# Performance work log

Hardware: AMD Instinct MI355X
Metric: run time of the kernel (lower is better)

The kernel has to match this reference:

```python
import jax, jax.numpy as jnp
import numpy as np

P = 8          # patch_size
DIM = 256      # embed dim
HEADS = 8
HEAD_DIM = DIM // HEADS
CH = 3
PATCH_DIM = CH * P * P  # 192
INNER = int(4.0 * DIM)  # 1024
SCALE = HEAD_DIM ** -0.5


def sine_pos_embedding(n, c, dtype=jnp.float32):
    # standard 1D sinusoidal position encoding, shape (n, c)
    pos = jnp.arange(n, dtype=jnp.float32)[:, None]            # (n,1)
    div = jnp.exp(jnp.arange(0, c, 2, dtype=jnp.float32) * (-np.log(10000.0) / c))
    pe = jnp.zeros((n, c), dtype=jnp.float32)
    pe = pe.at[:, 0::2].set(jnp.sin(pos * div))
    pe = pe.at[:, 1::2].set(jnp.cos(pos * div))
    return pe.astype(dtype)


def patchify(x):
    # (B,C,H,W) -> (B, n, p1*p2*C), matching 'b c (h p1) (w p2) -> b (h w) (p1 p2 c)'
    B, C, H, W = x.shape
    hp, wp = H // P, W // P
    x = x.reshape(B, C, hp, P, wp, P)
    x = x.transpose(0, 2, 4, 3, 5, 1)        # (B, hp, wp, p1, p2, C)
    return x.reshape(B, hp * wp, P * P * C)


def unpatchify(x, hp, wp):
    # (B, n, p1*p2*C) -> (B, C, H, W)
    B = x.shape[0]
    x = x.reshape(B, hp, wp, P, P, CH)
    x = x.transpose(0, 5, 1, 3, 2, 4)        # (B, C, hp, p1, wp, p2)
    return x.reshape(B, CH, hp * P, wp * P)


def setup_inputs() -> dict:
    key = jax.random.key(0)
    ks = jax.random.split(key, 16)
    B, H, W = 8, 256, 256
    s = 0.02
    img0 = jax.random.normal(ks[0], (B, CH, H, W), dtype=jnp.float32)
    img1 = jax.random.normal(ks[1], (B, CH, H, W), dtype=jnp.float32)
    mask = jax.random.randint(ks[2], (B, 1, H, W), 0, 2).astype(jnp.float32)
    return {
        "img0": img0,
        "img1": img1,
        "mask": mask,
        "w_patch": jax.random.normal(ks[3], (PATCH_DIM, DIM), jnp.float32) * s,
        "b_patch": jnp.zeros((DIM,), jnp.float32),
        "w_kv": jax.random.normal(ks[4], (DIM, 2 * DIM), jnp.float32) * s,
        "b_kv": jnp.zeros((2 * DIM,), jnp.float32),
        "w_qv": jax.random.normal(ks[5], (DIM, 2 * DIM), jnp.float32) * s,
        "b_qv": jnp.zeros((2 * DIM,), jnp.float32),
        "w_fc1": jax.random.normal(ks[6], (DIM, INNER), jnp.float32) * s,
        "b_fc1": jnp.zeros((INNER,), jnp.float32),
        "w_fc2": jax.random.normal(ks[7], (INNER, PATCH_DIM), jnp.float32) * s,
        "b_fc2": jnp.zeros((PATCH_DIM,), jnp.float32),
    }


def reference(img0, img1, mask, w_patch, b_patch, w_kv, b_kv, w_qv, b_qv,
              w_fc1, b_fc1, w_fc2, b_fc2):
    B, C, H, W = img0.shape
    hp, wp = H // P, W // P
    n = hp * wp

    x0 = patchify(img0) @ w_patch + b_patch   # (B, n, dim)
    x1 = patchify(img1) @ w_patch + b_patch
    pe = sine_pos_embedding(n, DIM)
    x0 = x0 + pe
    x1 = x1 + pe

    # img0 -> k, v
    kv = (x0 @ w_kv + b_kv).reshape(B, n, 2, HEADS, HEAD_DIM)
    kv = kv.transpose(2, 0, 3, 1, 4)          # (2, B, heads, n, hd)
    k, v = kv[0], kv[1]

    # img1 -> q (v1 unused in forward, matching torch code)
    qv = (x1 @ w_qv + b_qv).reshape(B, n, 2, DIM).transpose(2, 0, 1, 3)
    q = qv[0].reshape(B, n, HEADS, HEAD_DIM).transpose(0, 2, 1, 3)  # (B, heads, n, hd)

    dots = jnp.einsum('bhqd,bhkd->bhqk', q, k) * SCALE  # (B, heads, n, n)

    # mask: (B,1,H,W) -> per-patch sum -> binary -> additive bias over key dim
    msum = mask.reshape(B, 1, hp, P, wp, P).sum(axis=(3, 5)).reshape(B, 1, n)
    bias = jnp.where(msum > 0, 0.0, -100.0)[:, :, None, :]  # (B,1,1,n)

    attn = jax.nn.softmax(dots + bias, axis=-1)
    out = jnp.einsum('bhqk,bhkd->bhqd', attn, v)
    out = out.transpose(0, 2, 1, 3).reshape(B, n, DIM)

    # mlp2: Linear -> GELU(exact) -> Linear
    h = jax.nn.gelu(out @ w_fc1 + b_fc1, approximate=False)
    res = h @ w_fc2 + b_fc2                   # (B, n, patch_dim)

    return unpatchify(res, hp, wp)            # (B, C, H, W)
```

## Files before the change

kernel.cpp:

```cpp
#include <hip/hip_runtime.h>
#include <cstdint>
#include <cstddef>

typedef __bf16 bf16_t;
typedef __bf16 bf16x4 __attribute__((ext_vector_type(4)));
typedef __bf16 bf16x8 __attribute__((ext_vector_type(8)));
typedef float f32x4 __attribute__((ext_vector_type(4)));

__device__ __forceinline__ void gload_lds16(const bf16_t* g, bf16_t* l) {
  __builtin_amdgcn_global_load_lds((const __attribute__((address_space(1))) void*)g,
                                   (__attribute__((address_space(3))) void*)l,
                                   16, 0, 0);
}

__device__ __forceinline__ f32x4 mfma16(bf16x8 a, bf16x8 b, f32x4 c) {
  return __builtin_amdgcn_mfma_f32_16x16x32_bf16(a, b, c, 0, 0, 0);
}

__global__ __launch_bounds__(256)
void prep_all(const float* __restrict__ img0, const float* __restrict__ img1,
              const float* __restrict__ mask,
              const float* __restrict__ wp, const float* __restrict__ wkv,
              const float* __restrict__ wqv, const float* __restrict__ wfc1,
              const float* __restrict__ wfc2,
              bf16_t* __restrict__ xp0, bf16_t* __restrict__ xp1,
              float* __restrict__ pe, float* __restrict__ bias,
              bf16_t* __restrict__ wpT, bf16_t* __restrict__ wkvT,
              bf16_t* __restrict__ wqT, bf16_t* __restrict__ wfc1T,
              bf16_t* __restrict__ wfc2T) {
  int bid = blockIdx.x, tid = threadIdx.x;
  if (bid < 1536) {
    int imgsel = bid >= 768;
    int t = (bid - (imgsel ? 768 : 0)) * 256 + tid;
    const float* img = imgsel ? img1 : img0;
    bf16_t* xp = imgsel ? xp1 : xp0;
    int wpp = t & 31, p1 = (t >> 5) & 7, hp = (t >> 8) & 31, rest = t >> 13;
    int b = rest / 3, c = rest - b * 3;
    const float* src = img + (((size_t)(b * 3 + c) * 256 + hp * 8 + p1) * 256 + wpp * 8);
    float4 v0 = *(const float4*)src;
    float4 v1 = *(const float4*)(src + 4);
    int row = b * 1024 + hp * 32 + wpp;
    bf16_t* dst = xp + (size_t)row * 192 + p1 * 24 + c;
    dst[0]  = (bf16_t)v0.x; dst[3]  = (bf16_t)v0.y; dst[6]  = (bf16_t)v0.z; dst[9]  = (bf16_t)v0.w;
    dst[12] = (bf16_t)v1.x; dst[15] = (bf16_t)v1.y; dst[18] = (bf16_t)v1.z; dst[21] = (bf16_t)v1.w;
  } else if (bid < 4544) {
    int g = (bid - 1536) * 256 + tid;
    if (g < 49152) {
      int idx = g; int n = idx / 192, k = idx - n * 192;
      wpT[idx] = (bf16_t)wp[k * 256 + n];
    } else if (g < 180224) {
      int idx = g - 49152; int n = idx >> 8, k = idx & 255;
      wkvT[idx] = (bf16_t)wkv[k * 512 + n];
    } else if (g < 245760) {
      int idx = g - 180224; int n = idx >> 8, k = idx & 255;
      wqT[idx] = (bf16_t)wqv[k * 512 + n];
    } else if (g < 507904) {
      int idx = g - 245760; int n = idx >> 8, k = idx & 255;
      wfc1T[idx] = (bf16_t)wfc1[k * 1024 + n];
    } else if (g < 770048) {
      int idx = g - 507904; int n = idx >> 10, k = idx & 1023;
      wfc2T[idx] = (n < 192) ? (bf16_t)wfc2[k * 192 + n] : (bf16_t)0.0f;
    }
  } else if (bid < 5568) {
    int t = bid - 4544, c = tid;
    int i2 = c & ~1;
    float div = expf((float)i2 * (-9.210340371976184f / 256.0f));
    float arg = (float)t * div;
    pe[t * 256 + c] = (c & 1) ? cosf(arg) : sinf(arg);
  } else {
    int g = (bid - 5568) * 256 + tid;
    int b = g >> 10, t = g & 1023, hp = t >> 5, wpp = t & 31;
    const float* mp = mask + ((size_t)b * 256 + hp * 8) * 256 + wpp * 8;
    float s = 0.f;
    #pragma unroll
    for (int p1 = 0; p1 < 8; p1++) {
      float4 a = *(const float4*)(mp + p1 * 256);
      float4 c = *(const float4*)(mp + p1 * 256 + 4);
      s += a.x + a.y + a.z + a.w + c.x + c.y + c.z + c.w;
    }
    bias[g] = (s > 0.f) ? 0.f : -100.f;
  }
}

template<int EPI, int BN>
__global__ __launch_bounds__(256)
void gemm_bt(const bf16_t* __restrict__ A_, const bf16_t* __restrict__ A2,
             const bf16_t* __restrict__ Bt_, const bf16_t* __restrict__ Bt2,
             int M, int N, int K,
             const float* __restrict__ bias_, const float* __restrict__ bias2,
             const float* __restrict__ pe,
             bf16_t* __restrict__ out_b, bf16_t* __restrict__ out_b2,
             bf16_t* __restrict__ out_b3, float* __restrict__ out_f) {
  constexpr int NF = BN / 32;
  __shared__ bf16_t alds[4 * 64 * 8];
  __shared__ bf16_t blds[4 * BN * 8];
  const int tid = threadIdx.x;
  const int lane = tid & 63, wid = tid >> 6;
  const int ln15 = lane & 15, hi = lane >> 4;
  const int brow = blockIdx.x * 64;
  int bcol = blockIdx.y * BN;
  const bf16_t* A = A_;
  const bf16_t* Bt = Bt_;
  const float* bias = bias_;
  bool qpart = false;
  if (EPI == 0 && blockIdx.z) A = A2;
  if (EPI == 5 && blockIdx.y >= 4) {
    qpart = true; A = A2; Bt = Bt2; bias = bias2; bcol -= 512;
  }
  const int wr = wid >> 1, wc = wid & 1;

  f32x4 acc[2][NF];
  #pragma unroll
  for (int m = 0; m < 2; m++)
    #pragma unroll
    for (int n = 0; n < NF; n++) acc[m][n] = (f32x4){0.f, 0.f, 0.f, 0.f};

  for (int k0 = 0; k0 < K; k0 += 32) {
    {
      int c = tid; int row = c & 63; int kb = c >> 6;
      const bf16_t* g = A + (size_t)(brow + row) * K + k0 + kb * 8;
      gload_lds16(g, &alds[(wid * 64) * 8]);
    }
    #pragma unroll
    for (int s = 0; s < BN / 64; s++) {
      int c = tid + s * 256; int row = c & (BN - 1); int kb = c / BN;
      const bf16_t* g = Bt + (size_t)(bcol + row) * K + k0 + kb * 8;
      gload_lds16(g, &blds[(wid * 64 + s * 256) * 8]);
    }
    __syncthreads();
    bf16x8 af[2], bfr[NF];
    #pragma unroll
    for (int m = 0; m < 2; m++)
      af[m] = *(const bf16x8*)&alds[(hi * 64 + wr * 32 + m * 16 + ln15) * 8];
    #pragma unroll
    for (int n = 0; n < NF; n++)
      bfr[n] = *(const bf16x8*)&blds[(hi * BN + wc * (BN / 2) + n * 16 + ln15) * 8];
    #pragma unroll
    for (int m = 0; m < 2; m++)
      #pragma unroll
      for (int n = 0; n < NF; n++)
        acc[m][n] = mfma16(af[m], bfr[n], acc[m][n]);
    __syncthreads();
  }

  #pragma unroll
  for (int m = 0; m < 2; m++) {
    #pragma unroll
    for (int n = 0; n < NF; n++) {
      #pragma unroll
      for (int r = 0; r < 4; r++) {
        int grow = brow + wr * 32 + m * 16 + hi * 4 + r;
        int gcol = bcol + wc * (BN / 2) + n * 16 + ln15;
        float v = acc[m][n][r];
        if (EPI == 0) {
          v += bias[gcol] + pe[(grow & 1023) * 256 + gcol];
          bf16_t* outx = blockIdx.z ? out_b2 : out_b;
          outx[(size_t)grow * N + gcol] = (bf16_t)v;
        } else if (EPI == 5) {
          v += bias[gcol];
          int b = grow >> 10, t = grow & 1023;
          if (!qpart) {
            if (gcol < 256) {
              int h = gcol >> 5, d = gcol & 31;
              out_b[(((size_t)(b * 8 + h) * 1024 + t) << 5) + d] = (bf16_t)v;
            } else {
              int c2 = gcol - 256; int h = c2 >> 5, d = c2 & 31;
              out_b2[(((size_t)(b * 8 + h) * 32 + d) << 10) + t] = (bf16_t)v;
            }
          } else {
            v *= 0.17677669529663687f;
            int h = gcol >> 5, d = gcol & 31;
            out_b3[(((size_t)(b * 8 + h) * 1024 + t) << 5) + d] = (bf16_t)v;
          }
        } else if (EPI == 3) {
          v += bias[gcol];
          float gg = 0.5f * v * (1.0f + erff(v * 0.7071067811865476f));
          out_b[(size_t)grow * N + gcol] = (bf16_t)gg;
        } else if (EPI == 4) {
          if (gcol < 192) {
            v += bias[gcol];
            int b = grow >> 10, t = grow & 1023;
            int hp = t >> 5, wpp = t & 31;
            int p = gcol / 3; int c = gcol - p * 3;
            int p1 = p >> 3, p2 = p & 7;
            out_f[(((size_t)(b * 3 + c) * 256 + hp * 8 + p1) * 256) + wpp * 8 + p2] = v;
          }
        }
      }
    }
  }
}

__device__ __forceinline__ void attn_load(int kt, const bf16_t* kbase, const bf16_t* vbase,
                                          const float* bb, int ln15, int hi,
                                          bf16x8& kf0, bf16x8& kf1, bf16x8& vf0, bf16x8& vf1,
                                          f32x4& ba0, f32x4& ba1) {
  int k0 = kt * 32;
  kf0 = *(const bf16x8*)(kbase + (size_t)(k0 + ln15) * 32 + hi * 8);
  kf1 = *(const bf16x8*)(kbase + (size_t)(k0 + 16 + ln15) * 32 + hi * 8);
  vf0 = *(const bf16x8*)(vbase + (size_t)ln15 * 1024 + k0 + hi * 8);
  vf1 = *(const bf16x8*)(vbase + (size_t)(16 + ln15) * 1024 + k0 + hi * 8);
  ba0 = *(const f32x4*)(bb + k0 + hi * 4);
  ba1 = *(const f32x4*)(bb + k0 + 16 + hi * 4);
}

__device__ __forceinline__ void attn_step(bf16x8 kf0, bf16x8 kf1, bf16x8 vf0, bf16x8 vf1,
                                          f32x4 ba0, f32x4 ba1, bf16x8 qf,
                                          char* pwb, int ln15, int hi,
                                          float& lsum, f32x4& o0, f32x4& o1) {
  f32x4 s0 = mfma16(kf0, qf, ba0);
  f32x4 s1 = mfma16(kf1, qf, ba1);
  float e0 = __expf(s0[0]), e1 = __expf(s0[1]), e2 = __expf(s0[2]), e3 = __expf(s0[3]);
  float f0 = __expf(s1[0]), f1 = __expf(s1[1]), f2 = __expf(s1[2]), f3 = __expf(s1[3]);
  lsum += ((e0 + e1) + (e2 + e3)) + ((f0 + f1) + (f2 + f3));
  bf16x4 pk0, pk1;
  pk0[0] = (bf16_t)e0; pk0[1] = (bf16_t)e1; pk0[2] = (bf16_t)e2; pk0[3] = (bf16_t)e3;
  pk1[0] = (bf16_t)f0; pk1[1] = (bf16_t)f1; pk1[2] = (bf16_t)f2; pk1[3] = (bf16_t)f3;
  *(bf16x4*)(pwb + ln15 * 80 + hi * 8) = pk0;
  *(bf16x4*)(pwb + ln15 * 80 + 32 + hi * 8) = pk1;
  bf16x8 pf = *(const bf16x8*)(pwb + ln15 * 80 + hi * 16);
  o0 = mfma16(pf, vf0, o0);
  o1 = mfma16(pf, vf1, o1);
}

__global__ __launch_bounds__(256)
void attn_kernel(const bf16_t* __restrict__ q, const bf16_t* __restrict__ k,
                 const bf16_t* __restrict__ vt, const float* __restrict__ bias,
                 bf16_t* __restrict__ out) {
  __shared__ bf16_t plds[4 * 16 * 40];
  int tid = threadIdx.x;
  int lane = tid & 63, wid = tid >> 6, ln15 = lane & 15, hi = lane >> 4;
  int x = blockIdx.x & 7, idx = blockIdx.x >> 3;
  int qb = idx & 15;
  int bh = ((idx >> 4) << 3) | x;
  int b = bh >> 3, h = bh & 7;
  int qrow = qb * 64 + wid * 16 + ln15;
  bf16x8 qf = *(const bf16x8*)(q + ((size_t)bh * 1024 + qrow) * 32 + hi * 8);
  const bf16_t* kbase = k + (size_t)bh * 32768;
  const bf16_t* vbase = vt + (size_t)bh * 32768;
  const float* bb = bias + b * 1024;
  char* pwb = (char*)&plds[wid * 640];

  float lsum = 0.f;
  f32x4 o0 = (f32x4){0.f, 0.f, 0.f, 0.f}, o1 = o0;

  bf16x8 ka0, ka1, va0, va1, kb0, kb1, vb0, vb1;
  f32x4 aa0, aa1, ab0, ab1;
  attn_load(0, kbase, vbase, bb, ln15, hi, ka0, ka1, va0, va1, aa0, aa1);
  for (int kt = 0; kt < 32; kt += 2) {
    attn_load(kt + 1, kbase, vbase, bb, ln15, hi, kb0, kb1, vb0, vb1, ab0, ab1);
    attn_step(ka0, ka1, va0, va1, aa0, aa1, qf, pwb, ln15, hi, lsum, o0, o1);
    int ktn = (kt + 2 < 32) ? kt + 2 : 31;
    attn_load(ktn, kbase, vbase, bb, ln15, hi, ka0, ka1, va0, va1, aa0, aa1);
    attn_step(kb0, kb1, vb0, vb1, ab0, ab1, qf, pwb, ln15, hi, lsum, o0, o1);
  }

  lsum += __shfl_xor(lsum, 16);
  lsum += __shfl_xor(lsum, 32);
  #pragma unroll
  for (int r = 0; r < 4; r++) {
    float linv = 1.f / __shfl(lsum, hi * 4 + r);
    int qg = qb * 64 + wid * 16 + hi * 4 + r;
    size_t rowbase = ((size_t)b * 1024 + qg) * 256 + h * 32;
    out[rowbase + ln15] = (bf16_t)(o0[r] * linv);
    out[rowbase + 16 + ln15] = (bf16_t)(o1[r] * linv);
  }
}

extern "C" void kernel_launch(void* const* d_in, const int* in_sizes, int n_in,
                              void* d_out, int out_size, void* d_ws, size_t ws_size,
                              hipStream_t stream) {
  (void)in_sizes; (void)n_in; (void)out_size; (void)ws_size;
  const float* img0    = (const float*)d_in[0];
  const float* img1    = (const float*)d_in[1];
  const float* mask    = (const float*)d_in[2];
  const float* w_patch = (const float*)d_in[3];
  const float* b_patch = (const float*)d_in[4];
  const float* w_kv    = (const float*)d_in[5];
  const float* b_kv    = (const float*)d_in[6];
  const float* w_qv    = (const float*)d_in[7];
  const float* b_qv    = (const float*)d_in[8];
  const float* w_fc1   = (const float*)d_in[9];
  const float* b_fc1   = (const float*)d_in[10];
  const float* w_fc2   = (const float*)d_in[11];
  const float* b_fc2   = (const float*)d_in[12];
  float* out = (float*)d_out;

  char* ws = (char*)d_ws;
  float*  pe    = (float*)(ws + 0);
  float*  bias  = (float*)(ws + 1048576);
  bf16_t* wpT   = (bf16_t*)(ws + 1081344);
  bf16_t* wkvT  = (bf16_t*)(ws + 1179648);
  bf16_t* wqT   = (bf16_t*)(ws + 1441792);
  bf16_t* wfc1T = (bf16_t*)(ws + 1572864);
  bf16_t* wfc2T = (bf16_t*)(ws + 2097152);
  bf16_t* xp0   = (bf16_t*)(ws + 2621440);
  bf16_t* xp1   = (bf16_t*)(ws + 5767168);
  bf16_t* x0    = (bf16_t*)(ws + 8912896);
  bf16_t* x1    = (bf16_t*)(ws + 13107200);
  bf16_t* kbuf  = (bf16_t*)(ws + 17301504);
  bf16_t* vtbuf = (bf16_t*)(ws + 21495808);
  bf16_t* qbuf  = (bf16_t*)(ws + 25690112);
  bf16_t* aout  = (bf16_t*)(ws + 29884416);
  bf16_t* hbuf  = (bf16_t*)(ws + 34078720);

  prep_all<<<5600, 256, 0, stream>>>(img0, img1, mask, w_patch, w_kv, w_qv, w_fc1, w_fc2,
                                     xp0, xp1, pe, bias, wpT, wkvT, wqT, wfc1T, wfc2T);

  gemm_bt<0, 64><<<dim3(128, 4, 2), 256, 0, stream>>>(xp0, xp1, wpT, nullptr, 8192, 256, 192,
                                                      b_patch, nullptr, pe, x0, x1, nullptr, nullptr);
  gemm_bt<5, 128><<<dim3(128, 6), 256, 0, stream>>>(x0, x1, wkvT, wqT, 8192, 512, 256,
                                                    b_kv, b_qv, nullptr, kbuf, vtbuf, qbuf, nullptr);

  attn_kernel<<<1024, 256, 0, stream>>>(qbuf, kbuf, vtbuf, bias, aout);

  gemm_bt<3, 128><<<dim3(128, 8), 256, 0, stream>>>(aout, nullptr, wfc1T, nullptr, 8192, 1024, 256,
                                                    b_fc1, nullptr, nullptr, hbuf, nullptr, nullptr, nullptr);
  gemm_bt<4, 64><<<dim3(128, 4), 256, 0, stream>>>(hbuf, nullptr, wfc2T, nullptr, 8192, 256, 1024,
                                                   b_fc2, nullptr, nullptr, nullptr, nullptr, nullptr, out);
}
```

Measured before the change: 145.1 us.

## Rewrite attention with 32x32 MFMA, register P exchange, exp2 softmax; tile weight transposes

The attention kernel moves from 16x16x32 MFMA tiles with an LDS round-trip for the probability matrix to 32x32x16 MFMA tiles, 128 queries per block. The P operand is built in registers through cross-half lane shuffles, and the row sum comes from an MFMA against a ones vector. Softmax uses exp2 with log2e folded into the query scale and mask bias. Weight transposes in the prep kernel now go through a 64x64 shared-memory tile so global reads and writes are coalesced, and the block count drops. This removes LDS traffic and the scalar sum reductions, at the cost of extra MFMAs for the sums and higher register pressure.

```diff
diff --git a/kernel.cpp b/kernel.cpp
--- a/kernel.cpp
+++ b/kernel.cpp
@@ -3,9 +3,11 @@
 #include <cstddef>
 
 typedef __bf16 bf16_t;
+typedef uint32_t u32;
 typedef __bf16 bf16x4 __attribute__((ext_vector_type(4)));
 typedef __bf16 bf16x8 __attribute__((ext_vector_type(8)));
 typedef float f32x4 __attribute__((ext_vector_type(4)));
+typedef float f32x16 __attribute__((ext_vector_type(16)));
 
 __device__ __forceinline__ void gload_lds16(const bf16_t* g, bf16_t* l) {
   __builtin_amdgcn_global_load_lds((const __attribute__((address_space(1))) void*)g,
@@ -16,6 +18,11 @@
 __device__ __forceinline__ f32x4 mfma16(bf16x8 a, bf16x8 b, f32x4 c) {
   return __builtin_amdgcn_mfma_f32_16x16x32_bf16(a, b, c, 0, 0, 0);
 }
+__device__ __forceinline__ f32x16 mfma32(bf16x8 a, bf16x8 b, f32x16 c) {
+  return __builtin_amdgcn_mfma_f32_32x32x16_bf16(a, b, c, 0, 0, 0);
+}
+
+#define LOG2E 1.4426950408889634f
 
 __global__ __launch_bounds__(256)
 void prep_all(const float* __restrict__ img0, const float* __restrict__ img1,
@@ -28,6 +35,7 @@
               bf16_t* __restrict__ wpT, bf16_t* __restrict__ wkvT,
               bf16_t* __restrict__ wqT, bf16_t* __restrict__ wfc1T,
               bf16_t* __restrict__ wfc2T) {
+  __shared__ float tl[64 * 65];
   int bid = blockIdx.x, tid = threadIdx.x;
   if (bid < 1536) {
     int imgsel = bid >= 768;
@@ -43,32 +51,14 @@
     bf16_t* dst = xp + (size_t)row * 192 + p1 * 24 + c;
     dst[0]  = (bf16_t)v0.x; dst[3]  = (bf16_t)v0.y; dst[6]  = (bf16_t)v0.z; dst[9]  = (bf16_t)v0.w;
     dst[12] = (bf16_t)v1.x; dst[15] = (bf16_t)v1.y; dst[18] = (bf16_t)v1.z; dst[21] = (bf16_t)v1.w;
-  } else if (bid < 4544) {
-    int g = (bid - 1536) * 256 + tid;
-    if (g < 49152) {
-      int idx = g; int n = idx / 192, k = idx - n * 192;
-      wpT[idx] = (bf16_t)wp[k * 256 + n];
-    } else if (g < 180224) {
-      int idx = g - 49152; int n = idx >> 8, k = idx & 255;
-      wkvT[idx] = (bf16_t)wkv[k * 512 + n];
-    } else if (g < 245760) {
-      int idx = g - 180224; int n = idx >> 8, k = idx & 255;
-      wqT[idx] = (bf16_t)wqv[k * 512 + n];
-    } else if (g < 507904) {
-      int idx = g - 245760; int n = idx >> 8, k = idx & 255;
-      wfc1T[idx] = (bf16_t)wfc1[k * 1024 + n];
-    } else if (g < 770048) {
-      int idx = g - 507904; int n = idx >> 10, k = idx & 1023;
-      wfc2T[idx] = (n < 192) ? (bf16_t)wfc2[k * 192 + n] : (bf16_t)0.0f;
-    }
-  } else if (bid < 5568) {
-    int t = bid - 4544, c = tid;
+  } else if (bid < 2560) {
+    int t = bid - 1536, c = tid;
     int i2 = c & ~1;
     float div = expf((float)i2 * (-9.210340371976184f / 256.0f));
     float arg = (float)t * div;
     pe[t * 256 + c] = (c & 1) ? cosf(arg) : sinf(arg);
-  } else {
-    int g = (bid - 5568) * 256 + tid;
+  } else if (bid < 2592) {
+    int g = (bid - 2560) * 256 + tid;
     int b = g >> 10, t = g & 1023, hp = t >> 5, wpp = t & 31;
     const float* mp = mask + ((size_t)b * 256 + hp * 8) * 256 + wpp * 8;
     float s = 0.f;
@@ -78,7 +68,40 @@
       float4 c = *(const float4*)(mp + p1 * 256 + 4);
       s += a.x + a.y + a.z + a.w + c.x + c.y + c.z + c.w;
     }
-    bias[g] = (s > 0.f) ? 0.f : -100.f;
+    bias[g] = (s > 0.f) ? 0.f : (-100.f * LOG2E);
+  } else {
+    int i = bid - 2592;
+    const float* src; bf16_t* dst; int srcN, dstK, NT;
+    if (i >= 172) {
+      int j = i - 172;
+      bf16_t* p = wfc2T + 192 * 1024 + j * 8192 + tid * 32;
+      bf16x8 z;
+      #pragma unroll
+      for (int e = 0; e < 8; e++) z[e] = (bf16_t)0.0f;
+      *(bf16x8*)(p) = z; *(bf16x8*)(p + 8) = z;
+      *(bf16x8*)(p + 16) = z; *(bf16x8*)(p + 24) = z;
+      return;
+    }
+    if (i < 12)       { src = wp;   dst = wpT;   srcN = 256;  dstK = 192;  NT = 4; }
+    else if (i < 44)  { i -= 12;  src = wkv;  dst = wkvT;  srcN = 512;  dstK = 256;  NT = 8; }
+    else if (i < 60)  { i -= 44;  src = wqv;  dst = wqT;   srcN = 512;  dstK = 256;  NT = 4; }
+    else if (i < 124) { i -= 60;  src = wfc1; dst = wfc1T; srcN = 1024; dstK = 256;  NT = 16; }
+    else              { i -= 124; src = wfc2; dst = wfc2T; srcN = 192;  dstK = 1024; NT = 3; }
+    int kt = i / NT, nt = i - kt * NT;
+    #pragma unroll
+    for (int j = 0; j < 4; j++) {
+      int r = (tid >> 4) + 16 * j, c = (tid & 15) * 4;
+      float4 v = *(const float4*)(src + (size_t)(kt * 64 + r) * srcN + nt * 64 + c);
+      tl[r * 65 + c] = v.x; tl[r * 65 + c + 1] = v.y;
+      tl[r * 65 + c + 2] = v.z; tl[r * 65 + c + 3] = v.w;
+    }
+    __syncthreads();
+    #pragma unroll
+    for (int j = 0; j < 16; j++) {
+      int flat = tid + 256 * j;
+      int n_l = flat >> 6, k_l = flat & 63;
+      dst[(size_t)(nt * 64 + n_l) * dstK + kt * 64 + k_l] = (bf16_t)tl[k_l * 65 + n_l];
+    }
   }
 }
 
@@ -168,7 +191,7 @@
               out_b2[(((size_t)(b * 8 + h) * 32 + d) << 10) + t] = (bf16_t)v;
             }
           } else {
-            v *= 0.17677669529663687f;
+            v *= (0.17677669529663687f * LOG2E);
             int h = gcol >> 5, d = gcol & 31;
             out_b3[(((size_t)(b * 8 + h) * 1024 + t) << 5) + d] = (bf16_t)v;
           }
@@ -191,79 +214,98 @@
   }
 }
 
-__device__ __forceinline__ void attn_load(int kt, const bf16_t* kbase, const bf16_t* vbase,
-                                          const float* bb, int ln15, int hi,
-                                          bf16x8& kf0, bf16x8& kf1, bf16x8& vf0, bf16x8& vf1,
-                                          f32x4& ba0, f32x4& ba1) {
-  int k0 = kt * 32;
-  kf0 = *(const bf16x8*)(kbase + (size_t)(k0 + ln15) * 32 + hi * 8);
-  kf1 = *(const bf16x8*)(kbase + (size_t)(k0 + 16 + ln15) * 32 + hi * 8);
-  vf0 = *(const bf16x8*)(vbase + (size_t)ln15 * 1024 + k0 + hi * 8);
-  vf1 = *(const bf16x8*)(vbase + (size_t)(16 + ln15) * 1024 + k0 + hi * 8);
-  ba0 = *(const f32x4*)(bb + k0 + hi * 4);
-  ba1 = *(const f32x4*)(bb + k0 + 16 + hi * 4);
-}
-
-__device__ __forceinline__ void attn_step(bf16x8 kf0, bf16x8 kf1, bf16x8 vf0, bf16x8 vf1,
-                                          f32x4 ba0, f32x4 ba1, bf16x8 qf,
-                                          char* pwb, int ln15, int hi,
-                                          float& lsum, f32x4& o0, f32x4& o1) {
-  f32x4 s0 = mfma16(kf0, qf, ba0);
-  f32x4 s1 = mfma16(kf1, qf, ba1);
-  float e0 = __expf(s0[0]), e1 = __expf(s0[1]), e2 = __expf(s0[2]), e3 = __expf(s0[3]);
-  float f0 = __expf(s1[0]), f1 = __expf(s1[1]), f2 = __expf(s1[2]), f3 = __expf(s1[3]);
-  lsum += ((e0 + e1) + (e2 + e3)) + ((f0 + f1) + (f2 + f3));
-  bf16x4 pk0, pk1;
-  pk0[0] = (bf16_t)e0; pk0[1] = (bf16_t)e1; pk0[2] = (bf16_t)e2; pk0[3] = (bf16_t)e3;
-  pk1[0] = (bf16_t)f0; pk1[1] = (bf16_t)f1; pk1[2] = (bf16_t)f2; pk1[3] = (bf16_t)f3;
-  *(bf16x4*)(pwb + ln15 * 80 + hi * 8) = pk0;
-  *(bf16x4*)(pwb + ln15 * 80 + 32 + hi * 8) = pk1;
-  bf16x8 pf = *(const bf16x8*)(pwb + ln15 * 80 + hi * 16);
-  o0 = mfma16(pf, vf0, o0);
-  o1 = mfma16(pf, vf1, o1);
+struct Ld { bf16x8 kA, kB, vA, vB; f32x4 c0, c1, c2, c3; };
+
+__device__ __forceinline__ void ldstep(int k0, const bf16_t* kb, const bf16_t* vb,
+                                       const float* bb, int l31, int g, Ld& L) {
+  L.kA = *(const bf16x8*)(kb + (size_t)(k0 + l31) * 32 + g * 8);
+  L.kB = *(const bf16x8*)(kb + (size_t)(k0 + l31) * 32 + 16 + g * 8);
+  L.vA = *(const bf16x8*)(vb + (size_t)l31 * 1024 + k0 + g * 8);
+  L.vB = *(const bf16x8*)(vb + (size_t)l31 * 1024 + k0 + 16 + g * 8);
+  L.c0 = *(const f32x4*)(bb + k0 + 4 * g);
+  L.c1 = *(const f32x4*)(bb + k0 + 8 + 4 * g);
+  L.c2 = *(const f32x4*)(bb + k0 + 16 + 4 * g);
+  L.c3 = *(const f32x4*)(bb + k0 + 24 + 4 * g);
+}
+
+union PW { u32 w[4]; bf16x8 v; };
+
+__device__ __forceinline__ u32 pkbf(float a, float b) {
+  union { bf16_t h[2]; u32 w; } u;
+  u.h[0] = (bf16_t)a; u.h[1] = (bf16_t)b;
+  return u.w;
+}
+
+__device__ __forceinline__ void step(const Ld& L, bf16x8 qf0, bf16x8 qf1, int g,
+                                     f32x16& acc, f32x16& lacc, bf16x8 onesb) {
+  f32x16 S;
+  S[0] = L.c0[0]; S[1] = L.c0[1]; S[2] = L.c0[2]; S[3] = L.c0[3];
+  S[4] = L.c1[0]; S[5] = L.c1[1]; S[6] = L.c1[2]; S[7] = L.c1[3];
+  S[8] = L.c2[0]; S[9] = L.c2[1]; S[10] = L.c2[2]; S[11] = L.c2[3];
+  S[12] = L.c3[0]; S[13] = L.c3[1]; S[14] = L.c3[2]; S[15] = L.c3[3];
+  S = mfma32(L.kA, qf0, S);
+  S = mfma32(L.kB, qf1, S);
+  float p[16];
+  #pragma unroll
+  for (int r = 0; r < 16; r++) p[r] = exp2f(S[r]);
+  u32 w[8];
+  #pragma unroll
+  for (int j = 0; j < 8; j++) w[j] = pkbf(p[2 * j], p[2 * j + 1]);
+  u32 t0 = (u32)__shfl_xor((int)(g ? w[0] : w[2]), 32);
+  u32 t1 = (u32)__shfl_xor((int)(g ? w[1] : w[3]), 32);
+  u32 t2 = (u32)__shfl_xor((int)(g ? w[4] : w[6]), 32);
+  u32 t3 = (u32)__shfl_xor((int)(g ? w[5] : w[7]), 32);
+  PW A0, A1;
+  A0.w[0] = g ? t0 : w[0];  A0.w[1] = g ? t1 : w[1];
+  A0.w[2] = g ? w[2] : t0;  A0.w[3] = g ? w[3] : t1;
+  A1.w[0] = g ? t2 : w[4];  A1.w[1] = g ? t3 : w[5];
+  A1.w[2] = g ? w[6] : t2;  A1.w[3] = g ? w[7] : t3;
+  acc = mfma32(A0.v, L.vA, acc);
+  acc = mfma32(A1.v, L.vB, acc);
+  lacc = mfma32(A0.v, onesb, lacc);
+  lacc = mfma32(A1.v, onesb, lacc);
 }
 
 __global__ __launch_bounds__(256)
 void attn_kernel(const bf16_t* __restrict__ q, const bf16_t* __restrict__ k,
                  const bf16_t* __restrict__ vt, const float* __restrict__ bias,
                  bf16_t* __restrict__ out) {
-  __shared__ bf16_t plds[4 * 16 * 40];
-  int tid = threadIdx.x;
-  int lane = tid & 63, wid = tid >> 6, ln15 = lane & 15, hi = lane >> 4;
+  int tid = threadIdx.x, lane = tid & 63, wid = tid >> 6;
+  int l31 = lane & 31, g = lane >> 5;
   int x = blockIdx.x & 7, idx = blockIdx.x >> 3;
-  int qb = idx & 15;
-  int bh = ((idx >> 4) << 3) | x;
+  int qb = idx & 7;
+  int bh = ((idx >> 3) << 3) | x;
   int b = bh >> 3, h = bh & 7;
-  int qrow = qb * 64 + wid * 16 + ln15;
-  bf16x8 qf = *(const bf16x8*)(q + ((size_t)bh * 1024 + qrow) * 32 + hi * 8);
+  int q0 = qb * 128 + wid * 32;
+  const bf16_t* qp = q + ((size_t)bh * 1024 + q0 + l31) * 32;
+  bf16x8 qf0 = *(const bf16x8*)(qp + g * 8);
+  bf16x8 qf1 = *(const bf16x8*)(qp + 16 + g * 8);
   const bf16_t* kbase = k + (size_t)bh * 32768;
   const bf16_t* vbase = vt + (size_t)bh * 32768;
   const float* bb = bias + b * 1024;
-  char* pwb = (char*)&plds[wid * 640];
-
-  float lsum = 0.f;
-  f32x4 o0 = (f32x4){0.f, 0.f, 0.f, 0.f}, o1 = o0;
-
-  bf16x8 ka0, ka1, va0, va1, kb0, kb1, vb0, vb1;
-  f32x4 aa0, aa1, ab0, ab1;
-  attn_load(0, kbase, vbase, bb, ln15, hi, ka0, ka1, va0, va1, aa0, aa1);
+
+  bf16x8 onesb;
+  #pragma unroll
+  for (int e = 0; e < 8; e++) onesb[e] = (bf16_t)1.0f;
+  f32x16 acc, lacc;
+  #pragma unroll
+  for (int r = 0; r < 16; r++) { acc[r] = 0.f; lacc[r] = 0.f; }
+
+  Ld La, Lb;
+  ldstep(0, kbase, vbase, bb, l31, g, La);
   for (int kt = 0; kt < 32; kt += 2) {
-    attn_load(kt + 1, kbase, vbase, bb, ln15, hi, kb0, kb1, vb0, vb1, ab0, ab1);
-    attn_step(ka0, ka1, va0, va1, aa0, aa1, qf, pwb, ln15, hi, lsum, o0, o1);
-    int ktn = (kt + 2 < 32) ? kt + 2 : 31;
-    attn_load(ktn, kbase, vbase, bb, ln15, hi, ka0, ka1, va0, va1, aa0, aa1);
-    attn_step(kb0, kb1, vb0, vb1, ab0, ab1, qf, pwb, ln15, hi, lsum, o0, o1);
-  }
-
-  lsum += __shfl_xor(lsum, 16);
-  lsum += __shfl_xor(lsum, 32);
-  #pragma unroll
-  for (int r = 0; r < 4; r++) {
-    float linv = 1.f / __shfl(lsum, hi * 4 + r);
-    int qg = qb * 64 + wid * 16 + hi * 4 + r;
-    size_t rowbase = ((size_t)b * 1024 + qg) * 256 + h * 32;
-    out[rowbase + ln15] = (bf16_t)(o0[r] * linv);
-    out[rowbase + 16 + ln15] = (bf16_t)(o1[r] * linv);
+    ldstep((kt + 1) * 32, kbase, vbase, bb, l31, g, Lb);
+    step(La, qf0, qf1, g, acc, lacc, onesb);
+    int nx = (kt + 2 < 32) ? (kt + 2) * 32 : 31 * 32;
+    ldstep(nx, kbase, vbase, bb, l31, g, La);
+    step(Lb, qf0, qf1, g, acc, lacc, onesb);
+  }
+
+  #pragma unroll
+  for (int r = 0; r < 16; r++) {
+    int row = (r & 3) + 8 * (r >> 2) + 4 * g;
+    float o = acc[r] / lacc[r];
+    out[((size_t)b * 1024 + q0 + row) * 256 + h * 32 + l31] = (bf16_t)o;
   }
 }
 
@@ -304,7 +346,7 @@
   bf16_t* aout  = (bf16_t*)(ws + 29884416);
   bf16_t* hbuf  = (bf16_t*)(ws + 34078720);
 
-  prep_all<<<5600, 256, 0, stream>>>(img0, img1, mask, w_patch, w_kv, w_qv, w_fc1, w_fc2,
+  prep_all<<<2772, 256, 0, stream>>>(img0, img1, mask, w_patch, w_kv, w_qv, w_fc1, w_fc2,
                                      xp0, xp1, pe, bias, wpT, wkvT, wqT, wfc1T, wfc2T);
 
   gemm_bt<0, 64><<<dim3(128, 4, 2), 256, 0, stream>>>(xp0, xp1, wpT, nullptr, 8192, 256, 192,
@@ -312,7 +354,7 @@
   gemm_bt<5, 128><<<dim3(128, 6), 256, 0, stream>>>(x0, x1, wkvT, wqT, 8192, 512, 256,
                                                     b_kv, b_qv, nullptr, kbuf, vtbuf, qbuf, nullptr);
 
-  attn_kernel<<<1024, 256, 0, stream>>>(qbuf, kbuf, vtbuf, bias, aout);
+  attn_kernel<<<512, 256, 0, stream>>>(qbuf, kbuf, vtbuf, bias, aout);
 
   gemm_bt<3, 128><<<dim3(128, 8), 256, 0, stream>>>(aout, nullptr, wfc1T, nullptr, 8192, 1024, 256,
                                                     b_fc1, nullptr, nullptr, hbuf, nullptr, nullptr, nullptr);
```

Result: faster. 126.2 us (-13.0%).
